# Optimization experiments

Hardware: AMD Instinct MI355X
Metric: run time of the kernel (lower is better)

## Reference

```python
import jax, jax.numpy as jnp
import numpy as np
from jax import lax

B, Z, X, Y = 8, 4, 32, 32
N = Z * X * Y
REAL_SIZE = jnp.array([25.0, 25.0, 4.0], dtype=jnp.float32)
THRESHOLD = 0.5
CUTOFF = 2.0


def setup_inputs() -> dict:
    key = jax.random.key(0)
    k1, k2 = jax.random.split(key)
    pred = jax.random.normal(k1, (B, Z, X, Y, 10), dtype=jnp.float32)
    targ = jax.random.uniform(k2, (B, Z, X, Y, 10), dtype=jnp.float32)
    return {"pred": pred, "targ": targ}


def _grid():
    z, x, y = jnp.meshgrid(jnp.arange(Z), jnp.arange(X), jnp.arange(Y), indexing="ij")
    return jnp.stack([z, x, y], -1).reshape(N, 3).astype(jnp.float32)


def _nms_mask(adj0, a0):
    # Fixed-size masked version of the original iterative suppression:
    # adj0: [N,N] bool, strictly-upper-triangular 'closer than cutoff' graph
    # a0:   [N] bool, currently active (above-threshold) points in conf-desc order
    def step(state):
        a, _ = state
        m = adj0 & a[:, None] & a[None, :]
        mf = m.astype(jnp.float32)
        r = mf.sum(0)                              # restrain_tensor = DIS.sum(0)
        r = r - (r != 0).astype(jnp.float32) @ mf  # subtract suppressed suppressors
        return ((r == 0.0) & a, a.sum())
    def cond(state):
        a, prev = state
        return a.sum() != prev
    a, _ = lax.while_loop(cond, step, (a0, jnp.int32(-1)))
    return a


def _per_batch(pd_conf, pd_pos, pd_R, tg_conf, tg_pos, tg_R):
    # pd_conf/tg_conf: [N]; pd_pos/tg_pos: [N,3] normalized; pd_R/tg_R: [N,3,3]
    pd_active = pd_conf > THRESHOLD
    tg_active = tg_conf > THRESHOLD
    # sort predictions by confidence descending, inactive pushed to the end
    skey = jnp.where(pd_active, pd_conf, -jnp.inf)
    order = jnp.argsort(-skey)
    pd_pos = pd_pos[order]
    pd_R = pd_R[order]
    a0 = pd_active[order]
    # NMS in NORMALIZED coordinates (as in the original module: real_size scaling
    # is applied only AFTER argnms)
    d = jnp.sqrt(jnp.sum((pd_pos[:, None, :] - pd_pos[None, :, :]) ** 2, -1))  # [N,N]
    iu = jnp.arange(N)
    adj0 = (d < CUTOFF) & (iu[:, None] < iu[None, :])
    keep = lax.stop_gradient(_nms_mask(adj0, a0))
    # greedy matching in real coordinates
    pd_r = pd_pos * REAL_SIZE
    tg_r = tg_pos * REAL_SIZE
    dist = jnp.sqrt(jnp.sum((tg_r[:, None, :] - pd_r[None, :, :]) ** 2, -1))  # [N_tg, N_pd]
    within = (dist < CUTOFF) & tg_active[:, None] & keep[None, :]
    has = within.any(0)                 # pred j has at least one target within cutoff
    first_tg = jnp.argmax(within, 0)    # first (lowest-index) matching target per pred
    tp = has.sum().astype(jnp.int32)
    n_pd = keep.sum().astype(jnp.int32)
    n_tg = tg_active.sum().astype(jnp.int32)
    cm = jnp.stack([tp, n_pd - tp, n_tg - tp])  # [matched, unmatched_pred, unmatched_targ]
    # mean rotation-angle error over matched pairs (3 rotation rows each)
    tgRm = tg_R[first_tg]  # [N,3,3]
    cos = jnp.sum(pd_R * tgRm, -1) / (
        jnp.linalg.norm(pd_R, axis=-1) * jnp.linalg.norm(tgRm, axis=-1))
    ang = jnp.arccos(jnp.clip(cos, -1.0, 1.0)) / jnp.pi * 180.0  # [N,3]
    w = has.astype(jnp.float32)[:, None]
    ms = jnp.where(tp > 0,
                   jnp.sum(ang * w) / (3.0 * jnp.maximum(tp, 1).astype(jnp.float32)),
                   0.0)
    return cm, ms


def _forward(pred, targ):
    grid = _grid()
    zxy = jnp.array([Z, X, Y], dtype=jnp.float32)
    def fields(t, is_pred):
        conf = jax.nn.sigmoid(t[..., 0]) if is_pred else t[..., 0]
        conf = conf.reshape(B, N)
        pos = (t[..., 1:4].reshape(B, N, 3) + grid) / zxy  # (off + cell_idx)/ZXY
        rx = t[..., 4:7].reshape(B, N, 3)
        ry = t[..., 7:10].reshape(B, N, 3)
        R = jnp.stack([rx, ry, jnp.cross(rx, ry)], axis=-2)  # [B,N,3,3]
        return conf, pos, R
    pc, pp, pR = fields(pred, True)
    tc, tpos, tR = fields(targ, False)
    cm, ms = jax.vmap(_per_batch)(pc, pp, pR, tc, tpos, tR)
    return cm.reshape(B, 1, 1, 3), ms.reshape(B, 1, 1, 1).astype(jnp.float32)


def reference(pred, targ):
    return _forward(pred, targ)
```

## Files before the change

kernel.cpp:

```cpp
#include <hip/hip_runtime.h>
#include <math.h>

#define NB    8
#define NPTS  4096
#define NTH   1024
#define SPT   4
#define NFILT 16
#define MAXQ  64
#define MAXU  256
#define MAXK  256

__device__ __forceinline__ int blockReduceSumI(int v, int* scr, int tid) {
    #pragma unroll
    for (int o = 32; o > 0; o >>= 1) v += __shfl_down(v, o, 64);
    if ((tid & 63) == 0) scr[tid >> 6] = v;
    __syncthreads();
    if (tid == 0) {
        int s = 0;
        #pragma unroll
        for (int w = 0; w < NTH / 64; ++w) s += scr[w];
        scr[16] = s;
    }
    __syncthreads();
    return scr[16];
}

__device__ __forceinline__ float blockReduceSumF(float v, float* scr, int tid) {
    #pragma unroll
    for (int o = 32; o > 0; o >>= 1) v += __shfl_down(v, o, 64);
    if ((tid & 63) == 0) scr[tid >> 6] = v;
    __syncthreads();
    if (tid == 0) {
        float s = 0.0f;
        #pragma unroll
        for (int w = 0; w < NTH / 64; ++w) s += scr[w];
        scr[16] = s;
    }
    __syncthreads();
    return scr[16];
}

__device__ __forceinline__ float rowAngleDeg(float a0, float a1, float a2,
                                             float b0, float b1, float b2) {
    float dot = a0 * b0 + a1 * b1 + a2 * b2;
    float na = sqrtf(a0 * a0 + a1 * a1 + a2 * a2);
    float nb = sqrtf(b0 * b0 + b1 * b1 + b2 * b2);
    float c = dot / (na * nb);
    c = fminf(1.0f, fmaxf(-1.0f, c));
    return acosf(c) * 57.29577951308232f;
}

__global__ __launch_bounds__(NTH) void molan_kernel(const float* __restrict__ pred,
                                                    const float* __restrict__ targ,
                                                    float* __restrict__ out) {
    __shared__ int   scr_i[32];
    __shared__ float scr_f[32];
    __shared__ unsigned long long scr_m[16];
    __shared__ int   cnt[8];
    __shared__ unsigned long long f_key[NFILT];
    __shared__ float f_x[NFILT], f_y[NFILT], f_z[NFILT];
    __shared__ unsigned long long q_key[MAXQ];
    __shared__ float q_x[MAXQ], q_y[MAXQ], q_z[MAXQ];
    __shared__ unsigned long long u_key[MAXU];
    __shared__ float u_x[MAXU], u_y[MAXU], u_z[MAXU];
    __shared__ float k_x[MAXK], k_y[MAXK], k_z[MAXK];
    __shared__ int   k_idx[MAXK];
    __shared__ unsigned int k_match[MAXK];

    const int b = blockIdx.x;
    const int tid = threadIdx.x;
    const float* pb = pred + (size_t)b * NPTS * 10;
    const float* tb = targ + (size_t)b * NPTS * 10;

    unsigned long long key[SPT];
    bool  act[SPT];
    float cx[SPT], cy[SPT], cz[SPT];
    #pragma unroll
    for (int s = 0; s < SPT; ++s) {
        int n = 4 * tid + s;
        const float2* p2 = (const float2*)(pb + (size_t)n * 10);
        float2 A = p2[0];
        float2 Bv = p2[1];
        float conf = 1.0f / (1.0f + expf(-A.x));
        act[s] = conf > 0.5f;
        unsigned int u = ~(__float_as_uint(conf) | 0x80000000u);
        key[s] = ((unsigned long long)u << 32) | (unsigned int)n;
        float gz = (float)(n >> 10);
        float gx = (float)((n >> 5) & 31);
        float gy = (float)(n & 31);
        cx[s] = (A.y + gz) * 0.25f;
        cy[s] = (Bv.x + gx) * 0.03125f;
        cz[s] = (Bv.y + gy) * 0.03125f;
    }
    bool  t_act[SPT];
    float t_x[SPT], t_y[SPT], t_z[SPT];
    int loc_ntg = 0;
    #pragma unroll
    for (int s = 0; s < SPT; ++s) {
        int n = 4 * tid + s;
        const float2* p2 = (const float2*)(tb + (size_t)n * 10);
        float2 A = p2[0];
        float2 Bv = p2[1];
        bool a = A.x > 0.5f;
        t_act[s] = a;
        if (a) ++loc_ntg;
        float gz = (float)(n >> 10);
        float gx = (float)((n >> 5) & 31);
        float gy = (float)(n & 31);
        t_x[s] = (A.y + gz) * 0.25f * 25.0f;
        t_y[s] = (Bv.x + gx) * 0.03125f * 25.0f;
        t_z[s] = (Bv.y + gy) * 0.03125f * 4.0f;
    }

    int loc = 0;
    #pragma unroll
    for (int s = 0; s < SPT; ++s) loc += act[s] ? 1 : 0;
    int cur = blockReduceSumI(loc, scr_i, tid);
    int prev = -1;
    while (cur != prev) {
        if (tid == 0) cnt[0] = 0;
        __syncthreads();
        {
            unsigned long long bk = ~0ull;
            float bx = 0.f, by = 0.f, bz = 0.f;
            #pragma unroll
            for (int s = 0; s < SPT; ++s)
                if (act[s] && key[s] < bk) { bk = key[s]; bx = cx[s]; by = cy[s]; bz = cz[s]; }
            #pragma unroll
            for (int o = 32; o > 0; o >>= 1) {
                unsigned long long ok = __shfl_xor(bk, o, 64);
                float ox = __shfl_xor(bx, o, 64);
                float oy = __shfl_xor(by, o, 64);
                float oz = __shfl_xor(bz, o, 64);
                if (ok < bk) { bk = ok; bx = ox; by = oy; bz = oz; }
            }
            if ((tid & 63) == 0 && bk != ~0ull) {
                int e = atomicAdd(&cnt[0], 1);
                f_key[e] = bk; f_x[e] = bx; f_y[e] = by; f_z[e] = bz;
            }
        }
        __syncthreads();
        const int F = cnt[0];

        bool sflag[SPT], pend[SPT];
        int pending = 0;
        #pragma unroll
        for (int s = 0; s < SPT; ++s) {
            sflag[s] = false; pend[s] = false;
            if (!act[s]) continue;
            bool found = false;
            for (int f = 0; f < F; ++f) {
                if (f_key[f] < key[s]) {
                    float dx = f_x[f] - cx[s], dy = f_y[f] - cy[s], dz = f_z[f] - cz[s];
                    if (dx * dx + dy * dy + dz * dz < 4.0f) { found = true; break; }
                }
            }
            if (found) sflag[s] = true;
            else { pend[s] = true; ++pending; }
        }
        while (true) {
            int more = blockReduceSumI(pending, scr_i, tid);
            if (more == 0) break;
            if (tid == 0) cnt[1] = 0;
            __syncthreads();
            int qe[SPT];
            #pragma unroll
            for (int s = 0; s < SPT; ++s) {
                qe[s] = -1;
                if (pend[s]) {
                    int e = atomicAdd(&cnt[1], 1);
                    if (e < MAXQ) {
                        q_key[e] = key[s]; q_x[e] = cx[s]; q_y[e] = cy[s]; q_z[e] = cz[s];
                        qe[s] = e; pend[s] = false; --pending;
                    }
                }
            }
            __syncthreads();
            const int Q = min(cnt[1], MAXQ);
            unsigned long long mask = 0;
            for (int e = 0; e < Q; ++e) {
                unsigned long long qk = q_key[e];
                float qx = q_x[e], qy = q_y[e], qz = q_z[e];
                bool hit = false;
                #pragma unroll
                for (int s = 0; s < SPT; ++s) {
                    if (act[s] && key[s] < qk) {
                        float dx = cx[s] - qx, dy = cy[s] - qy, dz = cz[s] - qz;
                        if (dx * dx + dy * dy + dz * dz < 4.0f) hit = true;
                    }
                }
                if (hit) mask |= (1ull << e);
            }
            #pragma unroll
            for (int o = 32; o > 0; o >>= 1) mask |= __shfl_xor(mask, o, 64);
            if ((tid & 63) == 0) scr_m[tid >> 6] = mask;
            __syncthreads();
            unsigned long long full = 0;
            #pragma unroll
            for (int w = 0; w < NTH / 64; ++w) full |= scr_m[w];
            #pragma unroll
            for (int s = 0; s < SPT; ++s)
                if (qe[s] >= 0) sflag[s] = (full >> qe[s]) & 1ull;
            __syncthreads();
        }

        bool upend[SPT], supp[SPT];
        int up = 0;
        #pragma unroll
        for (int s = 0; s < SPT; ++s) {
            upend[s] = act[s] && !sflag[s];
            up += upend[s] ? 1 : 0;
            supp[s] = false;
        }
        while (true) {
            int more = blockReduceSumI(up, scr_i, tid);
            if (more == 0) break;
            if (tid == 0) cnt[2] = 0;
            __syncthreads();
            #pragma unroll
            for (int s = 0; s < SPT; ++s) {
                if (upend[s]) {
                    int e = atomicAdd(&cnt[2], 1);
                    if (e < MAXU) {
                        u_key[e] = key[s]; u_x[e] = cx[s]; u_y[e] = cy[s]; u_z[e] = cz[s];
                        upend[s] = false; --up;
                    }
                }
            }
            __syncthreads();
            const int Ku = min(cnt[2], MAXU);
            #pragma unroll
            for (int s = 0; s < SPT; ++s) {
                if (!act[s] || supp[s]) continue;
                for (int e = 0; e < Ku; ++e) {
                    if (u_key[e] < key[s]) {
                        float dx = u_x[e] - cx[s], dy = u_y[e] - cy[s], dz = u_z[e] - cz[s];
                        if (dx * dx + dy * dy + dz * dz < 4.0f) { supp[s] = true; break; }
                    }
                }
            }
            __syncthreads();
        }
        loc = 0;
        #pragma unroll
        for (int s = 0; s < SPT; ++s) {
            if (act[s] && supp[s]) act[s] = false;
            loc += act[s] ? 1 : 0;
        }
        prev = cur;
        cur = blockReduceSumI(loc, scr_i, tid);
    }
    const int n_pd = cur;

    bool kpend[SPT];
    int kp = 0;
    #pragma unroll
    for (int s = 0; s < SPT; ++s) { kpend[s] = act[s]; kp += act[s] ? 1 : 0; }
    int loc_tp = 0;
    float loc_ang = 0.0f;
    while (true) {
        int more = blockReduceSumI(kp, scr_i, tid);
        if (more == 0) break;
        if (tid == 0) cnt[3] = 0;
        __syncthreads();
        #pragma unroll
        for (int s = 0; s < SPT; ++s) {
            if (kpend[s]) {
                int e = atomicAdd(&cnt[3], 1);
                if (e < MAXK) {
                    k_x[e] = cx[s] * 25.0f; k_y[e] = cy[s] * 25.0f; k_z[e] = cz[s] * 4.0f;
                    k_idx[e] = 4 * tid + s;
                    k_match[e] = 0xFFFFFFFFu;
                    kpend[s] = false; --kp;
                }
            }
        }
        __syncthreads();
        const int K = min(cnt[3], MAXK);
        #pragma unroll
        for (int s = 0; s < SPT; ++s) {
            if (!t_act[s]) continue;
            int n = 4 * tid + s;
            float tx = t_x[s], ty = t_y[s], tz = t_z[s];
            for (int e = 0; e < K; ++e) {
                float dx = tx - k_x[e], dy = ty - k_y[e], dz = tz - k_z[e];
                if (dx * dx + dy * dy + dz * dz < 4.0f)
                    atomicMin(&k_match[e], (unsigned int)n);
            }
        }
        __syncthreads();
        if (tid < K) {
            unsigned int m = k_match[tid];
            if (m != 0xFFFFFFFFu) {
                ++loc_tp;
                const float2* pr = (const float2*)(pb + (size_t)k_idx[tid] * 10 + 4);
                float2 p0 = pr[0], p1 = pr[1], p2v = pr[2];
                float ax0 = p0.x, ax1 = p0.y, ax2 = p1.x;
                float ay0 = p1.y, ay1 = p2v.x, ay2 = p2v.y;
                float az0 = ax1 * ay2 - ax2 * ay1;
                float az1 = ax2 * ay0 - ax0 * ay2;
                float az2 = ax0 * ay1 - ax1 * ay0;
                const float2* tr = (const float2*)(tb + (size_t)m * 10 + 4);
                float2 t0 = tr[0], t1 = tr[1], t2v = tr[2];
                float bx0 = t0.x, bx1 = t0.y, bx2 = t1.x;
                float by0 = t1.y, by1 = t2v.x, by2 = t2v.y;
                float bz0 = bx1 * by2 - bx2 * by1;
                float bz1 = bx2 * by0 - bx0 * by2;
                float bz2 = bx0 * by1 - bx1 * by0;
                loc_ang += rowAngleDeg(ax0, ax1, ax2, bx0, bx1, bx2);
                loc_ang += rowAngleDeg(ay0, ay1, ay2, by0, by1, by2);
                loc_ang += rowAngleDeg(az0, az1, az2, bz0, bz1, bz2);
            }
        }
        __syncthreads();
    }

    int n_tg = blockReduceSumI(loc_ntg, scr_i, tid);
    int tp   = blockReduceSumI(loc_tp,  scr_i, tid);
    float angsum = blockReduceSumF(loc_ang, scr_f, tid);

    if (tid == 0) {
        out[b * 3 + 0] = (float)tp;
        out[b * 3 + 1] = (float)(n_pd - tp);
        out[b * 3 + 2] = (float)(n_tg - tp);
        out[NB * 3 + b] = (tp > 0) ? (angsum / (3.0f * (float)tp)) : 0.0f;
    }
}

extern "C" void kernel_launch(void* const* d_in, const int* in_sizes, int n_in,
                              void* d_out, int out_size, void* d_ws, size_t ws_size,
                              hipStream_t stream) {
    const float* pred = (const float*)d_in[0];
    const float* targ = (const float*)d_in[1];
    float* out = (float*)d_out;
    molan_kernel<<<dim3(NB), dim3(NTH), 0, stream>>>(pred, targ, out);
}
```

Before: 82.89 us.

## Stage coalesced float4 loads through LDS and remap point ownership per thread

Input loading now reads each batch's pred and targ data as coalesced float4 chunks into a shared staging buffer, double-buffered in registers. Each thread then picks its point's fields from LDS, and point ownership changes from 4*tid+s to tid+1024*s. The per-iteration filter build drops the atomic counter and its extra barrier by writing one slot per wavefront and always scanning all 16 slots. This is meant to replace strided 8-byte global loads with coalesced ones, at the cost of 40KB of LDS and more barriers. Writing empty slots with key ~0 relies on the comparison f_key < key never matching them.

```diff
diff --git a/kernel.cpp b/kernel.cpp
--- a/kernel.cpp
+++ b/kernel.cpp
@@ -53,6 +53,7 @@
 __global__ __launch_bounds__(NTH) void molan_kernel(const float* __restrict__ pred,
                                                     const float* __restrict__ targ,
                                                     float* __restrict__ out) {
+    __shared__ float4 stage[2560];
     __shared__ int   scr_i[32];
     __shared__ float scr_f[32];
     __shared__ unsigned long long scr_m[16];
@@ -71,45 +72,78 @@
     const int tid = threadIdx.x;
     const float* pb = pred + (size_t)b * NPTS * 10;
     const float* tb = targ + (size_t)b * NPTS * 10;
+    const float* sf = (const float*)stage;
 
     unsigned long long key[SPT];
     bool  act[SPT];
     float cx[SPT], cy[SPT], cz[SPT];
-    #pragma unroll
-    for (int s = 0; s < SPT; ++s) {
-        int n = 4 * tid + s;
-        const float2* p2 = (const float2*)(pb + (size_t)n * 10);
-        float2 A = p2[0];
-        float2 Bv = p2[1];
-        float conf = 1.0f / (1.0f + expf(-A.x));
-        act[s] = conf > 0.5f;
-        unsigned int u = ~(__float_as_uint(conf) | 0x80000000u);
-        key[s] = ((unsigned long long)u << 32) | (unsigned int)n;
-        float gz = (float)(n >> 10);
-        float gx = (float)((n >> 5) & 31);
-        float gy = (float)(n & 31);
-        cx[s] = (A.y + gz) * 0.25f;
-        cy[s] = (Bv.x + gx) * 0.03125f;
-        cz[s] = (Bv.y + gy) * 0.03125f;
+    {
+        const float4* g4 = (const float4*)pb;
+        float4 r0 = g4[tid], r1 = g4[tid + 1024], r2;
+        if (tid < 512) r2 = g4[tid + 2048];
+        for (int q = 0; q < 4; ++q) {
+            stage[tid] = r0;
+            stage[tid + 1024] = r1;
+            if (tid < 512) stage[tid + 2048] = r2;
+            __syncthreads();
+            if (q < 3) {
+                int base = 2560 * (q + 1);
+                r0 = g4[base + tid];
+                r1 = g4[base + tid + 1024];
+                if (tid < 512) r2 = g4[base + tid + 2048];
+            }
+            int n = tid + 1024 * q;
+            float conf_raw = sf[10 * tid + 0];
+            float oz = sf[10 * tid + 1];
+            float ox = sf[10 * tid + 2];
+            float oy = sf[10 * tid + 3];
+            float conf = 1.0f / (1.0f + expf(-conf_raw));
+            act[q] = conf > 0.5f;
+            unsigned int u = ~(__float_as_uint(conf) | 0x80000000u);
+            key[q] = ((unsigned long long)u << 32) | (unsigned int)n;
+            float gz = (float)(n >> 10);
+            float gx = (float)((n >> 5) & 31);
+            float gy = (float)(n & 31);
+            cx[q] = (oz + gz) * 0.25f;
+            cy[q] = (ox + gx) * 0.03125f;
+            cz[q] = (oy + gy) * 0.03125f;
+            __syncthreads();
+        }
     }
     bool  t_act[SPT];
     float t_x[SPT], t_y[SPT], t_z[SPT];
     int loc_ntg = 0;
-    #pragma unroll
-    for (int s = 0; s < SPT; ++s) {
-        int n = 4 * tid + s;
-        const float2* p2 = (const float2*)(tb + (size_t)n * 10);
-        float2 A = p2[0];
-        float2 Bv = p2[1];
-        bool a = A.x > 0.5f;
-        t_act[s] = a;
-        if (a) ++loc_ntg;
-        float gz = (float)(n >> 10);
-        float gx = (float)((n >> 5) & 31);
-        float gy = (float)(n & 31);
-        t_x[s] = (A.y + gz) * 0.25f * 25.0f;
-        t_y[s] = (Bv.x + gx) * 0.03125f * 25.0f;
-        t_z[s] = (Bv.y + gy) * 0.03125f * 4.0f;
+    {
+        const float4* g4 = (const float4*)tb;
+        float4 r0 = g4[tid], r1 = g4[tid + 1024], r2;
+        if (tid < 512) r2 = g4[tid + 2048];
+        for (int q = 0; q < 4; ++q) {
+            stage[tid] = r0;
+            stage[tid + 1024] = r1;
+            if (tid < 512) stage[tid + 2048] = r2;
+            __syncthreads();
+            if (q < 3) {
+                int base = 2560 * (q + 1);
+                r0 = g4[base + tid];
+                r1 = g4[base + tid + 1024];
+                if (tid < 512) r2 = g4[base + tid + 2048];
+            }
+            int n = tid + 1024 * q;
+            float tc = sf[10 * tid + 0];
+            float oz = sf[10 * tid + 1];
+            float ox = sf[10 * tid + 2];
+            float oy = sf[10 * tid + 3];
+            bool a = tc > 0.5f;
+            t_act[q] = a;
+            if (a) ++loc_ntg;
+            float gz = (float)(n >> 10);
+            float gx = (float)((n >> 5) & 31);
+            float gy = (float)(n & 31);
+            t_x[q] = (oz + gz) * 0.25f * 25.0f;
+            t_y[q] = (ox + gx) * 0.03125f * 25.0f;
+            t_z[q] = (oy + gy) * 0.03125f * 4.0f;
+            __syncthreads();
+        }
     }
 
     int loc = 0;
@@ -118,8 +152,6 @@
     int cur = blockReduceSumI(loc, scr_i, tid);
     int prev = -1;
     while (cur != prev) {
-        if (tid == 0) cnt[0] = 0;
-        __syncthreads();
         {
             unsigned long long bk = ~0ull;
             float bx = 0.f, by = 0.f, bz = 0.f;
@@ -134,13 +166,12 @@
                 float oz = __shfl_xor(bz, o, 64);
                 if (ok < bk) { bk = ok; bx = ox; by = oy; bz = oz; }
             }
-            if ((tid & 63) == 0 && bk != ~0ull) {
-                int e = atomicAdd(&cnt[0], 1);
-                f_key[e] = bk; f_x[e] = bx; f_y[e] = by; f_z[e] = bz;
-            }
-        }
-        __syncthreads();
-        const int F = cnt[0];
+            if ((tid & 63) == 0) {
+                int w = tid >> 6;
+                f_key[w] = bk; f_x[w] = bx; f_y[w] = by; f_z[w] = bz;
+            }
+        }
+        __syncthreads();
 
         bool sflag[SPT], pend[SPT];
         int pending = 0;
@@ -149,7 +180,7 @@
             sflag[s] = false; pend[s] = false;
             if (!act[s]) continue;
             bool found = false;
-            for (int f = 0; f < F; ++f) {
+            for (int f = 0; f < NFILT; ++f) {
                 if (f_key[f] < key[s]) {
                     float dx = f_x[f] - cx[s], dy = f_y[f] - cy[s], dz = f_z[f] - cz[s];
                     if (dx * dx + dy * dy + dz * dz < 4.0f) { found = true; break; }
@@ -269,7 +300,7 @@
                 int e = atomicAdd(&cnt[3], 1);
                 if (e < MAXK) {
                     k_x[e] = cx[s] * 25.0f; k_y[e] = cy[s] * 25.0f; k_z[e] = cz[s] * 4.0f;
-                    k_idx[e] = 4 * tid + s;
+                    k_idx[e] = tid + 1024 * s;
                     k_match[e] = 0xFFFFFFFFu;
                     kpend[s] = false; --kp;
                 }
@@ -280,7 +311,7 @@
         #pragma unroll
         for (int s = 0; s < SPT; ++s) {
             if (!t_act[s]) continue;
-            int n = 4 * tid + s;
+            int n = tid + 1024 * s;
             float tx = t_x[s], ty = t_y[s], tz = t_z[s];
             for (int e = 0; e < K; ++e) {
                 float dx = tx - k_x[e], dy = ty - k_y[e], dz = tz - k_z[e];
```

Measured after the change: 82.84 us. No clear change (-0.1%).
